# Performance work log

Measured on AMD Instinct MI355X. Metric: run time of the kernel, lower is better.

Reference implementation:

```python
import jax, jax.numpy as jnp
import numpy as np

DG, UF, Z, FD = 32, 4, 16, 16      # decoder grid, upsample factor, z bins, feat dim
H = W = DG * UF                     # 128 BEV resolution
S = 128                             # depth samples per ray
MLP_H = 32
X_MIN, X_MAX = -51.2, 51.2
Y_MIN, Y_MAX = -51.2, 51.2
Z_MIN, Z_MAX = -5.0, 3.0
D_MIN, D_MAX = 1.0, 50.0


def setup_inputs() -> dict:
    key = jax.random.key(0)
    ks = jax.random.split(key, 8)
    B, R, D = 2, 8192, 512
    out_dim = UF * UF * Z * FD
    s1 = 1.0 / np.sqrt(D); s2 = 1.0 / np.sqrt(FD); s3 = 1.0 / np.sqrt(MLP_H)
    return {
        'decoder_output': jax.random.normal(ks[0], (B, DG * DG, D), jnp.float32),
        'ray_origins': jax.random.normal(ks[1], (B, R, 3), jnp.float32),
        'ray_directions': jax.random.normal(ks[2], (B, R, 3), jnp.float32),
        'ln_g': jnp.ones((D,), jnp.float32),
        'ln_b': jnp.zeros((D,), jnp.float32),
        'W1': jax.random.uniform(ks[3], (D, out_dim), jnp.float32, -s1, s1),
        'b1': jnp.zeros((out_dim,), jnp.float32),
        'W2': jax.random.uniform(ks[4], (FD, MLP_H), jnp.float32, -s2, s2),
        'b2': jnp.zeros((MLP_H,), jnp.float32),
        'W3': jax.random.uniform(ks[5], (MLP_H, 1), jnp.float32, -s3, s3),
        'b3': jnp.zeros((1,), jnp.float32),
    }


def _build_nfg(dec, ln_g, ln_b, W1, b1):
    B = dec.shape[0]
    mu = dec.mean(-1, keepdims=True)
    var = dec.var(-1, keepdims=True)  # biased, matches torch LayerNorm
    x = (dec - mu) / jnp.sqrt(var + 1e-5) * ln_g + ln_b
    x = x @ W1 + b1
    x = x.reshape(B, DG, DG, UF, UF, Z, FD).transpose(0, 1, 3, 2, 4, 5, 6)
    x = x.reshape(B, H, W, Z, FD)
    return x.transpose(0, 4, 3, 1, 2)  # (B, F, Z, H, W)


def _trilinear_one(nfg_b, cw, ch, cd):
    # nfg_b: (F, Z, H, W); cw/ch/cd: (P,) in [-1,1] indexing W/H/Z resp.
    # align_corners=True mapping, zeros padding (mask OOB corners).
    fw = (cw + 1.0) * 0.5 * (W - 1)
    fh = (ch + 1.0) * 0.5 * (H - 1)
    fd = (cd + 1.0) * 0.5 * (Z - 1)
    w0 = jnp.floor(fw); h0 = jnp.floor(fh); d0 = jnp.floor(fd)
    tw = fw - w0; th = fh - h0; td = fd - d0
    out = jnp.zeros((nfg_b.shape[0], cw.shape[0]), nfg_b.dtype)
    for dd in (0, 1):
        for hh in (0, 1):
            for ww in (0, 1):
                di = d0 + dd; hi = h0 + hh; wi = w0 + ww
                wt = ((td if dd else 1.0 - td) * (th if hh else 1.0 - th)
                      * (tw if ww else 1.0 - tw))
                valid = ((di >= 0) & (di <= Z - 1) & (hi >= 0) & (hi <= H - 1)
                         & (wi >= 0) & (wi <= W - 1))
                dic = jnp.clip(di, 0, Z - 1).astype(jnp.int32)
                hic = jnp.clip(hi, 0, H - 1).astype(jnp.int32)
                wic = jnp.clip(wi, 0, W - 1).astype(jnp.int32)
                out = out + nfg_b[:, dic, hic, wic] * (wt * valid)
    return out  # (F, P)


def reference(decoder_output, ray_origins, ray_directions,
              ln_g, ln_b, W1, b1, W2, b2, W3, b3):
    nfg = _build_nfg(decoder_output, ln_g, ln_b, W1, b1)  # (B,F,Z,H,W)
    B, R, _ = ray_origins.shape
    t = jnp.linspace(0.0, 1.0, S, dtype=jnp.float32)
    depths = D_MIN + (D_MAX - D_MIN) * t                       # (S,)
    pts = ray_origins[:, :, None, :] + ray_directions[:, :, None, :] * depths[None, None, :, None]
    xn = 2.0 * (pts[..., 0] - X_MIN) / (X_MAX - X_MIN) - 1.0
    yn = 2.0 * (pts[..., 1] - Y_MIN) / (Y_MAX - Y_MIN) - 1.0
    zn = 2.0 * (pts[..., 2] - Z_MIN) / (Z_MAX - Z_MIN) - 1.0
    # torch grid_sample grid last dim = (x,y,z) -> (W,H,D); grid was stacked [y,x,z]
    cw = yn.reshape(B, -1); ch = xn.reshape(B, -1); cd = zn.reshape(B, -1)
    feats = jax.vmap(_trilinear_one)(nfg, cw, ch, cd)          # (B, F, R*S)
    feats = feats.transpose(0, 2, 1).reshape(B, R, S, FD)
    h = jax.nn.relu(feats @ W2 + b2)
    alpha = jax.nn.sigmoid((h @ W3 + b3)[..., 0])              # (B, R, S)
    oma = 1.0 - alpha + 1e-10
    trans = jnp.cumprod(
        jnp.concatenate([jnp.ones((B, R, 1), alpha.dtype), oma[..., :-1]], -1), -1)
    weights = alpha * trans
    pred_depths = (weights * depths[None, None, :]).sum(-1)    # (B, R)
    return pred_depths, weights, nfg
```

## Files before the change

### kernel.cpp

```cpp
#include <hip/hip_runtime.h>
#include <math.h>

#define DG   32
#define UF   4
#define ZB   16
#define FD   16
#define HH   128
#define WWID 128
#define SNUM 128
#define BATCH 2
#define RAYS  8192
#define NTOK  2048
#define DINP  512
#define ODIM  4096
#define MLPH  32

#define OUT_PRED_OFF 0
#define OUT_W_OFF    (BATCH*RAYS)
#define OUT_NFG_OFF  (OUT_W_OFF + BATCH*RAYS*SNUM)

typedef _Float16 half8 __attribute__((ext_vector_type(8)));
typedef _Float16 half4 __attribute__((ext_vector_type(4)));
typedef _Float16 h2 __attribute__((ext_vector_type(2)));
typedef float f32x4 __attribute__((ext_vector_type(4)));

#define GLDS16(gp, lp) \
    __builtin_amdgcn_global_load_lds((const __attribute__((address_space(1))) void*)(gp), \
                                     (__attribute__((address_space(3))) void*)(lp), 16, 0, 0)

__global__ __launch_bounds__(256) void prep_kernel(const float* __restrict__ dec,
                                                   const float* __restrict__ lng,
                                                   const float* __restrict__ lnb,
                                                   const float* __restrict__ W2,
                                                   const float* __restrict__ b2,
                                                   const float* __restrict__ W3,
                                                   const float* __restrict__ W1,
                                                   _Float16* __restrict__ Af,
                                                   _Float16* __restrict__ W1T,
                                                   _Float16* __restrict__ W2f,
                                                   float* __restrict__ b2f,
                                                   float* __restrict__ w3f) {
    int tid = threadIdx.x;
    if (blockIdx.x < NTOK) {
        int t = blockIdx.x;
        const float2* row = reinterpret_cast<const float2*>(dec + (size_t)t * DINP);
        float2 v = row[tid];

        __shared__ float red[4];
        __shared__ float stat[2];

        float s = v.x + v.y;
        #pragma unroll
        for (int o = 32; o > 0; o >>= 1) s += __shfl_down(s, o);
        if ((tid & 63) == 0) red[tid >> 6] = s;
        __syncthreads();
        if (tid == 0) stat[0] = (red[0] + red[1] + red[2] + red[3]) * (1.0f / DINP);
        __syncthreads();
        float mu = stat[0];

        float dx = v.x - mu, dy = v.y - mu;
        float q = dx * dx + dy * dy;
        #pragma unroll
        for (int o = 32; o > 0; o >>= 1) q += __shfl_down(q, o);
        if ((tid & 63) == 0) red[tid >> 6] = q;
        __syncthreads();
        if (tid == 0) {
            float var = (red[0] + red[1] + red[2] + red[3]) * (1.0f / DINP);
            stat[1] = 1.0f / sqrtf(var + 1e-5f);
        }
        __syncthreads();
        float rstd = stat[1];

        int c = 2 * tid;
        h2 o2;
        o2.x = (_Float16)(dx * rstd * lng[c]     + lnb[c]);
        o2.y = (_Float16)(dy * rstd * lng[c + 1] + lnb[c + 1]);
        *reinterpret_cast<h2*>(Af + (size_t)t * DINP + c) = o2;

        if (blockIdx.x == 0 && tid < 128) {
            int jt = tid >> 6, l = tid & 63;
            int sub = l & 15, g = l >> 4;
            #pragma unroll
            for (int e = 0; e < 4; ++e) {
                W2f[(jt * 64 + l) * 4 + e] = (_Float16)W2[(g * 4 + e) * MLPH + jt * 16 + sub];
                b2f[(jt * 64 + l) * 4 + e] = b2[jt * 16 + g * 4 + e];
                w3f[(jt * 64 + l) * 4 + e] = W3[jt * 16 + g * 4 + e];
            }
        }
    } else {
        __shared__ float st[64][65];
        int blk = blockIdx.x - NTOK;
        int c0 = (blk & 63) * 64;
        int k0 = (blk >> 6) * 64;
        {
            int r = tid >> 2, cq = (tid & 3) * 16;
            const float* src = W1 + (size_t)(k0 + r) * ODIM + c0 + cq;
            #pragma unroll
            for (int qq = 0; qq < 4; ++qq) {
                float4 v = *reinterpret_cast<const float4*>(src + qq * 4);
                st[r][cq + qq * 4 + 0] = v.x;
                st[r][cq + qq * 4 + 1] = v.y;
                st[r][cq + qq * 4 + 2] = v.z;
                st[r][cq + qq * 4 + 3] = v.w;
            }
        }
        __syncthreads();
        {
            int cc = tid >> 2, kq = (tid & 3) * 16;
            _Float16 tmp[16];
            #pragma unroll
            for (int i = 0; i < 16; ++i) tmp[i] = (_Float16)st[kq + i][cc];
            _Float16* dst = W1T + (size_t)(c0 + cc) * DINP + k0 + kq;
            *reinterpret_cast<half8*>(dst)     = *reinterpret_cast<half8*>(&tmp[0]);
            *reinterpret_cast<half8*>(dst + 8) = *reinterpret_cast<half8*>(&tmp[8]);
        }
    }
}

__global__ __launch_bounds__(256, 2) void gemm_mfma_kernel(
        const _Float16* __restrict__ Af, const _Float16* __restrict__ W1T,
        const float* __restrict__ bias, _Float16* __restrict__ gh) {
    __shared__ _Float16 As[128 * 32];
    __shared__ _Float16 Bs[128 * 32];

    int tid = threadIdx.x;
    int l = tid & 63, w = tid >> 6;
    int wr = w >> 1, wc = w & 1;
    int row0 = blockIdx.y * 128;
    int col0 = blockIdx.x * 128;

    const char* Ag0 = (const char*)Af + (size_t)(row0 + w * 32 + (l >> 2)) * (DINP * 2) + (l & 3) * 16;
    const char* Ag1 = Ag0 + 16 * (DINP * 2);
    const char* Bg0 = (const char*)W1T + (size_t)(col0 + w * 32 + (l >> 2)) * (DINP * 2) + (l & 3) * 16;
    const char* Bg1 = Bg0 + 16 * (DINP * 2);
    char* lA0 = (char*)As + w * 2048;
    char* lA1 = lA0 + 1024;
    char* lB0 = (char*)Bs + w * 2048;
    char* lB1 = lB0 + 1024;

    f32x4 acc[4][4] = {};

    for (int kk = 0; kk < DINP; kk += 32) {
        GLDS16(Ag0, lA0); GLDS16(Ag1, lA1);
        GLDS16(Bg0, lB0); GLDS16(Bg1, lB1);
        Ag0 += 64; Ag1 += 64; Bg0 += 64; Bg1 += 64;
        __syncthreads();

        half8 af[4], bf[4];
        #pragma unroll
        for (int m = 0; m < 4; ++m)
            af[m] = *reinterpret_cast<const half8*>(As + (wr * 64 + m * 16 + (l & 15)) * 32 + (l >> 4) * 8);
        #pragma unroll
        for (int n = 0; n < 4; ++n)
            bf[n] = *reinterpret_cast<const half8*>(Bs + (wc * 64 + n * 16 + (l & 15)) * 32 + (l >> 4) * 8);
        #pragma unroll
        for (int m = 0; m < 4; ++m)
            #pragma unroll
            for (int n = 0; n < 4; ++n)
                acc[m][n] = __builtin_amdgcn_mfma_f32_16x16x32_f16(af[m], bf[n], acc[m][n], 0, 0, 0);
        __syncthreads();
    }

    #pragma unroll
    for (int n = 0; n < 4; ++n) {
        int c = col0 + wc * 64 + n * 16 + (l & 15);
        float bv = bias[c];
        int f = c & 15, z = (c >> 4) & 15, v = (c >> 8) & 3, u = (c >> 10) & 3;
        #pragma unroll
        for (int m = 0; m < 4; ++m) {
            int rbase = row0 + wr * 64 + m * 16 + ((l >> 4) << 2);
            #pragma unroll
            for (int j = 0; j < 4; ++j) {
                int t = rbase + j;
                int bb = t >> 10;
                int g = t & 1023;
                int i = g >> 5, j2 = g & 31;
                int h = i * 4 + u, wq = j2 * 4 + v;
                size_t gaddr = ((((size_t)(bb * ZB + z) * HH + h) * WWID + wq) << 4) + f;
                gh[gaddr] = (_Float16)(acc[m][n][j] + bv);
            }
        }
    }
}

__device__ __forceinline__ void gather_feat(const _Float16* __restrict__ gb,
                                            float px, float py, float pz,
                                            h2* __restrict__ a) {
    float fw = (py * (1.0f / 51.2f) + 1.0f) * 63.5f;
    float fh = (px * (1.0f / 51.2f) + 1.0f) * 63.5f;
    float fd = (pz + 5.0f) * (0.25f * 7.5f);
    float w0f = floorf(fw), h0f = floorf(fh), d0f = floorf(fd);
    float tw = fw - w0f, th = fh - h0f, td = fd - d0f;
    int w0 = (int)w0f, h0 = (int)h0f, d0 = (int)d0f;

    float aw0 = (w0 >= 0 && w0 <= WWID - 1) ? (1.0f - tw) : 0.0f;
    float aw1 = (w0 + 1 >= 0 && w0 + 1 <= WWID - 1) ? tw : 0.0f;
    float ah0 = (h0 >= 0 && h0 <= HH - 1) ? (1.0f - th) : 0.0f;
    float ah1 = (h0 + 1 >= 0 && h0 + 1 <= HH - 1) ? th : 0.0f;
    float ad0 = (d0 >= 0 && d0 <= ZB - 1) ? (1.0f - td) : 0.0f;
    float ad1 = (d0 + 1 >= 0 && d0 + 1 <= ZB - 1) ? td : 0.0f;

    if ((ad0 + ad1) * (ah0 + ah1) * (aw0 + aw1) <= 0.0f) return;

    int w0c = min(max(w0, 0), WWID - 1), w1c = min(max(w0 + 1, 0), WWID - 1);
    int h0c = min(max(h0, 0), HH - 1),   h1c = min(max(h0 + 1, 0), HH - 1);
    int d0c = min(max(d0, 0), ZB - 1),   d1c = min(max(d0 + 1, 0), ZB - 1);

    int od0 = d0c * (HH * WWID * FD), od1 = d1c * (HH * WWID * FD);
    int oh0 = h0c * (WWID * FD),      oh1 = h1c * (WWID * FD);
    int ow0 = w0c * FD,               ow1 = w1c * FD;

#define CORNER(OFF, WF) do { \
        const uint4* cp_ = reinterpret_cast<const uint4*>(gb + (OFF)); \
        uint4 A_ = cp_[0], B_ = cp_[1]; \
        _Float16 wh_ = (_Float16)(WF); \
        h2 w2_ = {wh_, wh_}; \
        a[0] += __builtin_bit_cast(h2, A_.x) * w2_; \
        a[1] += __builtin_bit_cast(h2, A_.y) * w2_; \
        a[2] += __builtin_bit_cast(h2, A_.z) * w2_; \
        a[3] += __builtin_bit_cast(h2, A_.w) * w2_; \
        a[4] += __builtin_bit_cast(h2, B_.x) * w2_; \
        a[5] += __builtin_bit_cast(h2, B_.y) * w2_; \
        a[6] += __builtin_bit_cast(h2, B_.z) * w2_; \
        a[7] += __builtin_bit_cast(h2, B_.w) * w2_; \
    } while (0)

    CORNER(od0 + oh0 + ow0, ad0 * ah0 * aw0);
    CORNER(od0 + oh0 + ow1, ad0 * ah0 * aw1);
    CORNER(od0 + oh1 + ow0, ad0 * ah1 * aw0);
    CORNER(od0 + oh1 + ow1, ad0 * ah1 * aw1);
    CORNER(od1 + oh0 + ow0, ad1 * ah0 * aw0);
    CORNER(od1 + oh0 + ow1, ad1 * ah0 * aw1);
    CORNER(od1 + oh1 + ow0, ad1 * ah1 * aw0);
    CORNER(od1 + oh1 + ow1, ad1 * ah1 * aw1);
#undef CORNER
}

#define SF 24
#define RAYBLK (BATCH * RAYS / 4)
__global__ __launch_bounds__(256) void consume_kernel(
        const float* __restrict__ orig, const float* __restrict__ dirs,
        const _Float16* __restrict__ gh,
        const _Float16* __restrict__ W2f, const float* __restrict__ b2f,
        const float* __restrict__ w3f, const float* __restrict__ b3,
        float* __restrict__ pred_out, float* __restrict__ w_out,
        float* __restrict__ nfg) {
    __shared__ __align__(16) char smem[4 * 128 * SF * 2];
    int tid = threadIdx.x;
    int bx = blockIdx.x;

    if ((bx & 1) == 0) {
        _Float16* featLDS = reinterpret_cast<_Float16*>(smem);
        int lane = tid & 63, wvid = tid >> 6;
        int ray = (bx >> 1) * 4 + wvid;
        int bb = ray >> 13;

        _Float16* FL = &featLDS[wvid * 128 * SF];

        const float* o3 = orig + (size_t)ray * 3;
        const float* d3 = dirs + (size_t)ray * 3;
        float ox = o3[0], oy = o3[1], oz = o3[2];
        float dx = d3[0], dy = d3[1], dz = d3[2];

        const _Float16* gb = gh + (size_t)bb * (ZB * HH * WWID * FD);

        float t0 = 1.0f + 49.0f * ((float)lane * (1.0f / 127.0f));
        float t1 = 1.0f + 49.0f * ((float)(lane + 64) * (1.0f / 127.0f));

        h2 acc0[8] = {}, acc1[8] = {};
        gather_feat(gb, ox + dx * t0, oy + dy * t0, oz + dz * t0, acc0);
        gather_feat(gb, ox + dx * t1, oy + dy * t1, oz + dz * t1, acc1);

        {
            uint4 p0, p1;
            p0.x = __builtin_bit_cast(unsigned int, acc0[0]);
            p0.y = __builtin_bit_cast(unsigned int, acc0[1]);
            p0.z = __builtin_bit_cast(unsigned int, acc0[2]);
            p0.w = __builtin_bit_cast(unsigned int, acc0[3]);
            p1.x = __builtin_bit_cast(unsigned int, acc0[4]);
            p1.y = __builtin_bit_cast(unsigned int, acc0[5]);
            p1.z = __builtin_bit_cast(unsigned int, acc0[6]);
            p1.w = __builtin_bit_cast(unsigned int, acc0[7]);
            *reinterpret_cast<uint4*>(FL + lane * SF)     = p0;
            *reinterpret_cast<uint4*>(FL + lane * SF + 8) = p1;
            uint4 q0, q1;
            q0.x = __builtin_bit_cast(unsigned int, acc1[0]);
            q0.y = __builtin_bit_cast(unsigned int, acc1[1]);
            q0.z = __builtin_bit_cast(unsigned int, acc1[2]);
            q0.w = __builtin_bit_cast(unsigned int, acc1[3]);
            q1.x = __builtin_bit_cast(unsigned int, acc1[4]);
            q1.y = __builtin_bit_cast(unsigned int, acc1[5]);
            q1.z = __builtin_bit_cast(unsigned int, acc1[6]);
            q1.w = __builtin_bit_cast(unsigned int, acc1[7]);
            *reinterpret_cast<uint4*>(FL + (lane + 64) * SF)     = q0;
            *reinterpret_cast<uint4*>(FL + (lane + 64) * SF + 8) = q1;
        }

        half4 Af0 = *reinterpret_cast<const half4*>(W2f + lane * 4);
        half4 Af1 = *reinterpret_cast<const half4*>(W2f + (64 + lane) * 4);
        f32x4 b20 = *reinterpret_cast<const f32x4*>(b2f + lane * 4);
        f32x4 b21 = *reinterpret_cast<const f32x4*>(b2f + (64 + lane) * 4);
        f32x4 w30 = *reinterpret_cast<const f32x4*>(w3f + lane * 4);
        f32x4 w31 = *reinterpret_cast<const f32x4*>(w3f + (64 + lane) * 4);
        float b3v = b3[0];

        float at[8];
        #pragma unroll
        for (int tt = 0; tt < 8; ++tt) {
            half4 bfrag = *reinterpret_cast<const half4*>(
                FL + (tt * 16 + (lane & 15)) * SF + (lane >> 4) * 4);
            f32x4 c0 = __builtin_amdgcn_mfma_f32_16x16x16f16(Af0, bfrag, b20, 0, 0, 0);
            f32x4 c1 = __builtin_amdgcn_mfma_f32_16x16x16f16(Af1, bfrag, b21, 0, 0, 0);
            float p = 0.0f;
            #pragma unroll
            for (int r = 0; r < 4; ++r) {
                p = fmaf(fmaxf(c0[r], 0.0f), w30[r], p);
                p = fmaf(fmaxf(c1[r], 0.0f), w31[r], p);
            }
            p += __shfl_xor(p, 16);
            p += __shfl_xor(p, 32);
            at[tt] = p;
        }
        int g2 = lane >> 4;
        float aS0 = at[0];
        aS0 = (g2 == 1) ? at[1] : aS0;
        aS0 = (g2 == 2) ? at[2] : aS0;
        aS0 = (g2 == 3) ? at[3] : aS0;
        float aS1 = at[4];
        aS1 = (g2 == 1) ? at[5] : aS1;
        aS1 = (g2 == 2) ? at[6] : aS1;
        aS1 = (g2 == 3) ? at[7] : aS1;
        aS0 += b3v; aS1 += b3v;

        float alpha0 = 1.0f / (1.0f + __expf(-aS0));
        float alpha1 = 1.0f / (1.0f + __expf(-aS1));
        float oma0 = 1.0f - alpha0 + 1e-10f;
        float oma1 = 1.0f - alpha1 + 1e-10f;

        float P = oma0;
        #pragma unroll
        for (int off = 1; off < 64; off <<= 1) {
            float u = __shfl_up(P, off);
            if (lane >= off) P *= u;
        }
        float T64 = __shfl(P, 63);
        float Q = oma1;
        #pragma unroll
        for (int off = 1; off < 64; off <<= 1) {
            float u = __shfl_up(Q, off);
            if (lane >= off) Q *= u;
        }
        float e0 = __shfl_up(P, 1);
        if (lane == 0) e0 = 1.0f;
        float e1 = __shfl_up(Q, 1);
        e1 = (lane == 0) ? T64 : e1 * T64;

        float w0 = alpha0 * e0;
        float w1 = alpha1 * e1;
        w_out[(size_t)ray * SNUM + lane] = w0;
        w_out[(size_t)ray * SNUM + 64 + lane] = w1;

        float pv = w0 * t0 + w1 * t1;
        #pragma unroll
        for (int o = 32; o > 0; o >>= 1) pv += __shfl_xor(pv, o);
        if (lane == 0) pred_out[ray] = pv;
    } else {
        float* sl = reinterpret_cast<float*>(smem);
        int blk = bx >> 1;
        int bb = blk >> 11, z = (blk >> 7) & 15, h = blk & 127;
        const uint4* src = reinterpret_cast<const uint4*>(gh + (size_t)blk * 2048);
        uint4 v = src[tid];
        int wv = tid >> 1, fb = (tid & 1) * 8;
        h2 p0 = __builtin_bit_cast(h2, v.x);
        h2 p1 = __builtin_bit_cast(h2, v.y);
        h2 p2 = __builtin_bit_cast(h2, v.z);
        h2 p3 = __builtin_bit_cast(h2, v.w);
        float* sr = &sl[wv * 17 + fb];
        sr[0] = (float)p0.x; sr[1] = (float)p0.y;
        sr[2] = (float)p1.x; sr[3] = (float)p1.y;
        sr[4] = (float)p2.x; sr[5] = (float)p2.y;
        sr[6] = (float)p3.x; sr[7] = (float)p3.y;
        __syncthreads();
        int f = tid >> 4, w0 = (tid & 15) * 8;
        float* dst = nfg + (((size_t)(bb * FD + f) * ZB + z) * (HH * WWID)) + h * WWID + w0;
        float4 o0, o1;
        o0.x = sl[(w0 + 0) * 17 + f]; o0.y = sl[(w0 + 1) * 17 + f];
        o0.z = sl[(w0 + 2) * 17 + f]; o0.w = sl[(w0 + 3) * 17 + f];
        o1.x = sl[(w0 + 4) * 17 + f]; o1.y = sl[(w0 + 5) * 17 + f];
        o1.z = sl[(w0 + 6) * 17 + f]; o1.w = sl[(w0 + 7) * 17 + f];
        *reinterpret_cast<float4*>(dst) = o0;
        *reinterpret_cast<float4*>(dst + 4) = o1;
    }
}

extern "C" void kernel_launch(void* const* d_in, const int* in_sizes, int n_in,
                              void* d_out, int out_size, void* d_ws, size_t ws_size,
                              hipStream_t stream) {
    const float* dec = (const float*)d_in[0];
    const float* ro  = (const float*)d_in[1];
    const float* rd  = (const float*)d_in[2];
    const float* lng = (const float*)d_in[3];
    const float* lnb = (const float*)d_in[4];
    const float* W1  = (const float*)d_in[5];
    const float* b1  = (const float*)d_in[6];
    const float* W2  = (const float*)d_in[7];
    const float* b2  = (const float*)d_in[8];
    const float* W3  = (const float*)d_in[9];
    const float* b3  = (const float*)d_in[10];

    float* out = (float*)d_out;
    char*  wsb = (char*)d_ws;
    _Float16* Af  = (_Float16*)wsb;
    _Float16* W1T = (_Float16*)(wsb + (2u << 20));
    _Float16* gh  = (_Float16*)(wsb + (6u << 20));
    _Float16* W2f = (_Float16*)(wsb + (23u << 20));
    float*    b2f = (float*)(wsb + (23u << 20) + 4096);
    float*    w3f = (float*)(wsb + (23u << 20) + 8192);

    prep_kernel<<<NTOK + (ODIM / 64) * (DINP / 64), 256, 0, stream>>>(
        dec, lng, lnb, W2, b2, W3, W1, Af, W1T, W2f, b2f, w3f);

    dim3 gg(ODIM / 128, NTOK / 128);
    gemm_mfma_kernel<<<gg, 256, 0, stream>>>(Af, W1T, b1, gh);

    consume_kernel<<<2 * RAYBLK, 256, 0, stream>>>(ro, rd, gh, W2f, b2f, w3f, b3,
                                                   out + OUT_PRED_OFF, out + OUT_W_OFF,
                                                   out + OUT_NFG_OFF);
}
```

Baseline: 71.85 us.

## Split NFG transpose into own kernel, pair W-corner loads, halve feature LDS

The interleaved consume kernel is split into a dedicated ray kernel and a separate transpose kernel that writes the NFG output, launched after it. Trilinear gathering now loads the two W-neighbour corners as one contiguous 64-byte read from a clamped base index, with the weights remapped at the borders. Features for the two sample halves are staged through a half-size LDS buffer in turn, which lowers LDS use per block and may raise occupancy. The cost is an extra kernel launch and no more overlap between the transpose and ray work.

Result: faster. 63.57 us (-11.5%).

```diff
diff --git a/kernel.cpp b/kernel.cpp
--- a/kernel.cpp
+++ b/kernel.cpp
@@ -183,6 +183,36 @@
     }
 }
 
+__global__ __launch_bounds__(256) void tp_kernel(const _Float16* __restrict__ gh,
+                                                 float* __restrict__ nfg) {
+    int blk = blockIdx.x;
+    int bb = blk >> 11, z = (blk >> 7) & 15, h = blk & 127;
+    __shared__ float sl[128 * 17];
+    int tid = threadIdx.x;
+    const uint4* src = reinterpret_cast<const uint4*>(gh + (size_t)blk * 2048);
+    uint4 v = src[tid];
+    int wv = tid >> 1, fb = (tid & 1) * 8;
+    h2 p0 = __builtin_bit_cast(h2, v.x);
+    h2 p1 = __builtin_bit_cast(h2, v.y);
+    h2 p2 = __builtin_bit_cast(h2, v.z);
+    h2 p3 = __builtin_bit_cast(h2, v.w);
+    float* sr = &sl[wv * 17 + fb];
+    sr[0] = (float)p0.x; sr[1] = (float)p0.y;
+    sr[2] = (float)p1.x; sr[3] = (float)p1.y;
+    sr[4] = (float)p2.x; sr[5] = (float)p2.y;
+    sr[6] = (float)p3.x; sr[7] = (float)p3.y;
+    __syncthreads();
+    int f = tid >> 4, w0 = (tid & 15) * 8;
+    float* dst = nfg + (((size_t)(bb * FD + f) * ZB + z) * (HH * WWID)) + h * WWID + w0;
+    float4 o0, o1;
+    o0.x = sl[(w0 + 0) * 17 + f]; o0.y = sl[(w0 + 1) * 17 + f];
+    o0.z = sl[(w0 + 2) * 17 + f]; o0.w = sl[(w0 + 3) * 17 + f];
+    o1.x = sl[(w0 + 4) * 17 + f]; o1.y = sl[(w0 + 5) * 17 + f];
+    o1.z = sl[(w0 + 6) * 17 + f]; o1.w = sl[(w0 + 7) * 17 + f];
+    *reinterpret_cast<float4*>(dst) = o0;
+    *reinterpret_cast<float4*>(dst + 4) = o1;
+}
+
 __device__ __forceinline__ void gather_feat(const _Float16* __restrict__ gb,
                                             float px, float py, float pz,
                                             h2* __restrict__ a) {
@@ -202,111 +232,100 @@
 
     if ((ad0 + ad1) * (ah0 + ah1) * (aw0 + aw1) <= 0.0f) return;
 
-    int w0c = min(max(w0, 0), WWID - 1), w1c = min(max(w0 + 1, 0), WWID - 1);
     int h0c = min(max(h0, 0), HH - 1),   h1c = min(max(h0 + 1, 0), HH - 1);
     int d0c = min(max(d0, 0), ZB - 1),   d1c = min(max(d0 + 1, 0), ZB - 1);
+    int wb = min(max(w0, 0), WWID - 2);
+    float ws0 = (wb == w0) ? aw0 : ((wb == w0 + 1) ? aw1 : 0.0f);
+    float ws1 = (wb == w0) ? aw1 : ((wb == w0 - 1) ? aw0 : 0.0f);
 
     int od0 = d0c * (HH * WWID * FD), od1 = d1c * (HH * WWID * FD);
     int oh0 = h0c * (WWID * FD),      oh1 = h1c * (WWID * FD);
-    int ow0 = w0c * FD,               ow1 = w1c * FD;
-
-#define CORNER(OFF, WF) do { \
+    int ow  = wb * FD;
+
+#define CPAIR(OFF, WDH) do { \
         const uint4* cp_ = reinterpret_cast<const uint4*>(gb + (OFF)); \
-        uint4 A_ = cp_[0], B_ = cp_[1]; \
-        _Float16 wh_ = (_Float16)(WF); \
-        h2 w2_ = {wh_, wh_}; \
-        a[0] += __builtin_bit_cast(h2, A_.x) * w2_; \
-        a[1] += __builtin_bit_cast(h2, A_.y) * w2_; \
-        a[2] += __builtin_bit_cast(h2, A_.z) * w2_; \
-        a[3] += __builtin_bit_cast(h2, A_.w) * w2_; \
-        a[4] += __builtin_bit_cast(h2, B_.x) * w2_; \
-        a[5] += __builtin_bit_cast(h2, B_.y) * w2_; \
-        a[6] += __builtin_bit_cast(h2, B_.z) * w2_; \
-        a[7] += __builtin_bit_cast(h2, B_.w) * w2_; \
+        uint4 A_ = cp_[0], B_ = cp_[1], C_ = cp_[2], D_ = cp_[3]; \
+        _Float16 u0_ = (_Float16)((WDH) * ws0); \
+        _Float16 u1_ = (_Float16)((WDH) * ws1); \
+        h2 W0_ = {u0_, u0_}; h2 W1_ = {u1_, u1_}; \
+        a[0] += __builtin_bit_cast(h2, A_.x) * W0_; \
+        a[1] += __builtin_bit_cast(h2, A_.y) * W0_; \
+        a[2] += __builtin_bit_cast(h2, A_.z) * W0_; \
+        a[3] += __builtin_bit_cast(h2, A_.w) * W0_; \
+        a[4] += __builtin_bit_cast(h2, B_.x) * W0_; \
+        a[5] += __builtin_bit_cast(h2, B_.y) * W0_; \
+        a[6] += __builtin_bit_cast(h2, B_.z) * W0_; \
+        a[7] += __builtin_bit_cast(h2, B_.w) * W0_; \
+        a[0] += __builtin_bit_cast(h2, C_.x) * W1_; \
+        a[1] += __builtin_bit_cast(h2, C_.y) * W1_; \
+        a[2] += __builtin_bit_cast(h2, C_.z) * W1_; \
+        a[3] += __builtin_bit_cast(h2, C_.w) * W1_; \
+        a[4] += __builtin_bit_cast(h2, D_.x) * W1_; \
+        a[5] += __builtin_bit_cast(h2, D_.y) * W1_; \
+        a[6] += __builtin_bit_cast(h2, D_.z) * W1_; \
+        a[7] += __builtin_bit_cast(h2, D_.w) * W1_; \
     } while (0)
 
-    CORNER(od0 + oh0 + ow0, ad0 * ah0 * aw0);
-    CORNER(od0 + oh0 + ow1, ad0 * ah0 * aw1);
-    CORNER(od0 + oh1 + ow0, ad0 * ah1 * aw0);
-    CORNER(od0 + oh1 + ow1, ad0 * ah1 * aw1);
-    CORNER(od1 + oh0 + ow0, ad1 * ah0 * aw0);
-    CORNER(od1 + oh0 + ow1, ad1 * ah0 * aw1);
-    CORNER(od1 + oh1 + ow0, ad1 * ah1 * aw0);
-    CORNER(od1 + oh1 + ow1, ad1 * ah1 * aw1);
-#undef CORNER
+    CPAIR(od0 + oh0 + ow, ad0 * ah0);
+    CPAIR(od0 + oh1 + ow, ad0 * ah1);
+    CPAIR(od1 + oh0 + ow, ad1 * ah0);
+    CPAIR(od1 + oh1 + ow, ad1 * ah1);
+#undef CPAIR
 }
 
 #define SF 24
-#define RAYBLK (BATCH * RAYS / 4)
-__global__ __launch_bounds__(256) void consume_kernel(
+__global__ __launch_bounds__(256) void ray_fused_kernel(
         const float* __restrict__ orig, const float* __restrict__ dirs,
         const _Float16* __restrict__ gh,
         const _Float16* __restrict__ W2f, const float* __restrict__ b2f,
         const float* __restrict__ w3f, const float* __restrict__ b3,
-        float* __restrict__ pred_out, float* __restrict__ w_out,
-        float* __restrict__ nfg) {
-    __shared__ __align__(16) char smem[4 * 128 * SF * 2];
+        float* __restrict__ pred_out, float* __restrict__ w_out) {
     int tid = threadIdx.x;
-    int bx = blockIdx.x;
-
-    if ((bx & 1) == 0) {
-        _Float16* featLDS = reinterpret_cast<_Float16*>(smem);
-        int lane = tid & 63, wvid = tid >> 6;
-        int ray = (bx >> 1) * 4 + wvid;
-        int bb = ray >> 13;
-
-        _Float16* FL = &featLDS[wvid * 128 * SF];
-
-        const float* o3 = orig + (size_t)ray * 3;
-        const float* d3 = dirs + (size_t)ray * 3;
-        float ox = o3[0], oy = o3[1], oz = o3[2];
-        float dx = d3[0], dy = d3[1], dz = d3[2];
-
-        const _Float16* gb = gh + (size_t)bb * (ZB * HH * WWID * FD);
-
-        float t0 = 1.0f + 49.0f * ((float)lane * (1.0f / 127.0f));
-        float t1 = 1.0f + 49.0f * ((float)(lane + 64) * (1.0f / 127.0f));
-
-        h2 acc0[8] = {}, acc1[8] = {};
-        gather_feat(gb, ox + dx * t0, oy + dy * t0, oz + dz * t0, acc0);
-        gather_feat(gb, ox + dx * t1, oy + dy * t1, oz + dz * t1, acc1);
-
-        {
-            uint4 p0, p1;
-            p0.x = __builtin_bit_cast(unsigned int, acc0[0]);
-            p0.y = __builtin_bit_cast(unsigned int, acc0[1]);
-            p0.z = __builtin_bit_cast(unsigned int, acc0[2]);
-            p0.w = __builtin_bit_cast(unsigned int, acc0[3]);
-            p1.x = __builtin_bit_cast(unsigned int, acc0[4]);
-            p1.y = __builtin_bit_cast(unsigned int, acc0[5]);
-            p1.z = __builtin_bit_cast(unsigned int, acc0[6]);
-            p1.w = __builtin_bit_cast(unsigned int, acc0[7]);
-            *reinterpret_cast<uint4*>(FL + lane * SF)     = p0;
-            *reinterpret_cast<uint4*>(FL + lane * SF + 8) = p1;
-            uint4 q0, q1;
-            q0.x = __builtin_bit_cast(unsigned int, acc1[0]);
-            q0.y = __builtin_bit_cast(unsigned int, acc1[1]);
-            q0.z = __builtin_bit_cast(unsigned int, acc1[2]);
-            q0.w = __builtin_bit_cast(unsigned int, acc1[3]);
-            q1.x = __builtin_bit_cast(unsigned int, acc1[4]);
-            q1.y = __builtin_bit_cast(unsigned int, acc1[5]);
-            q1.z = __builtin_bit_cast(unsigned int, acc1[6]);
-            q1.w = __builtin_bit_cast(unsigned int, acc1[7]);
-            *reinterpret_cast<uint4*>(FL + (lane + 64) * SF)     = q0;
-            *reinterpret_cast<uint4*>(FL + (lane + 64) * SF + 8) = q1;
-        }
-
-        half4 Af0 = *reinterpret_cast<const half4*>(W2f + lane * 4);
-        half4 Af1 = *reinterpret_cast<const half4*>(W2f + (64 + lane) * 4);
-        f32x4 b20 = *reinterpret_cast<const f32x4*>(b2f + lane * 4);
-        f32x4 b21 = *reinterpret_cast<const f32x4*>(b2f + (64 + lane) * 4);
-        f32x4 w30 = *reinterpret_cast<const f32x4*>(w3f + lane * 4);
-        f32x4 w31 = *reinterpret_cast<const f32x4*>(w3f + (64 + lane) * 4);
-        float b3v = b3[0];
-
-        float at[8];
-        #pragma unroll
-        for (int tt = 0; tt < 8; ++tt) {
+    int lane = tid & 63, wvid = tid >> 6;
+    int ray = blockIdx.x * 4 + wvid;
+    int bb = ray >> 13;
+
+    __shared__ _Float16 featLDS[4 * 64 * SF];
+    _Float16* FL = &featLDS[wvid * 64 * SF];
+
+    const float* o3 = orig + (size_t)ray * 3;
+    const float* d3 = dirs + (size_t)ray * 3;
+    float ox = o3[0], oy = o3[1], oz = o3[2];
+    float dx = d3[0], dy = d3[1], dz = d3[2];
+
+    const _Float16* gb = gh + (size_t)bb * (ZB * HH * WWID * FD);
+
+    float t0 = 1.0f + 49.0f * ((float)lane * (1.0f / 127.0f));
+    float t1 = 1.0f + 49.0f * ((float)(lane + 64) * (1.0f / 127.0f));
+
+    h2 acc0[8] = {}, acc1[8] = {};
+    gather_feat(gb, ox + dx * t0, oy + dy * t0, oz + dz * t0, acc0);
+    gather_feat(gb, ox + dx * t1, oy + dy * t1, oz + dz * t1, acc1);
+
+    half4 Af0 = *reinterpret_cast<const half4*>(W2f + lane * 4);
+    half4 Af1 = *reinterpret_cast<const half4*>(W2f + (64 + lane) * 4);
+    f32x4 b20 = *reinterpret_cast<const f32x4*>(b2f + lane * 4);
+    f32x4 b21 = *reinterpret_cast<const f32x4*>(b2f + (64 + lane) * 4);
+    f32x4 w30 = *reinterpret_cast<const f32x4*>(w3f + lane * 4);
+    f32x4 w31 = *reinterpret_cast<const f32x4*>(w3f + (64 + lane) * 4);
+    float b3v = b3[0];
+
+    float at[8];
+
+    {
+        uint4 p0, p1;
+        p0.x = __builtin_bit_cast(unsigned int, acc0[0]);
+        p0.y = __builtin_bit_cast(unsigned int, acc0[1]);
+        p0.z = __builtin_bit_cast(unsigned int, acc0[2]);
+        p0.w = __builtin_bit_cast(unsigned int, acc0[3]);
+        p1.x = __builtin_bit_cast(unsigned int, acc0[4]);
+        p1.y = __builtin_bit_cast(unsigned int, acc0[5]);
+        p1.z = __builtin_bit_cast(unsigned int, acc0[6]);
+        p1.w = __builtin_bit_cast(unsigned int, acc0[7]);
+        *reinterpret_cast<uint4*>(FL + lane * SF)     = p0;
+        *reinterpret_cast<uint4*>(FL + lane * SF + 8) = p1;
+        #pragma unroll
+        for (int tt = 0; tt < 4; ++tt) {
             half4 bfrag = *reinterpret_cast<const half4*>(
                 FL + (tt * 16 + (lane & 15)) * SF + (lane >> 4) * 4);
             f32x4 c0 = __builtin_amdgcn_mfma_f32_16x16x16f16(Af0, bfrag, b20, 0, 0, 0);
@@ -321,76 +340,80 @@
             p += __shfl_xor(p, 32);
             at[tt] = p;
         }
-        int g2 = lane >> 4;
-        float aS0 = at[0];
-        aS0 = (g2 == 1) ? at[1] : aS0;
-        aS0 = (g2 == 2) ? at[2] : aS0;
-        aS0 = (g2 == 3) ? at[3] : aS0;
-        float aS1 = at[4];
-        aS1 = (g2 == 1) ? at[5] : aS1;
-        aS1 = (g2 == 2) ? at[6] : aS1;
-        aS1 = (g2 == 3) ? at[7] : aS1;
-        aS0 += b3v; aS1 += b3v;
-
-        float alpha0 = 1.0f / (1.0f + __expf(-aS0));
-        float alpha1 = 1.0f / (1.0f + __expf(-aS1));
-        float oma0 = 1.0f - alpha0 + 1e-10f;
-        float oma1 = 1.0f - alpha1 + 1e-10f;
-
-        float P = oma0;
-        #pragma unroll
-        for (int off = 1; off < 64; off <<= 1) {
-            float u = __shfl_up(P, off);
-            if (lane >= off) P *= u;
-        }
-        float T64 = __shfl(P, 63);
-        float Q = oma1;
-        #pragma unroll
-        for (int off = 1; off < 64; off <<= 1) {
-            float u = __shfl_up(Q, off);
-            if (lane >= off) Q *= u;
-        }
-        float e0 = __shfl_up(P, 1);
-        if (lane == 0) e0 = 1.0f;
-        float e1 = __shfl_up(Q, 1);
-        e1 = (lane == 0) ? T64 : e1 * T64;
-
-        float w0 = alpha0 * e0;
-        float w1 = alpha1 * e1;
-        w_out[(size_t)ray * SNUM + lane] = w0;
-        w_out[(size_t)ray * SNUM + 64 + lane] = w1;
-
-        float pv = w0 * t0 + w1 * t1;
-        #pragma unroll
-        for (int o = 32; o > 0; o >>= 1) pv += __shfl_xor(pv, o);
-        if (lane == 0) pred_out[ray] = pv;
-    } else {
-        float* sl = reinterpret_cast<float*>(smem);
-        int blk = bx >> 1;
-        int bb = blk >> 11, z = (blk >> 7) & 15, h = blk & 127;
-        const uint4* src = reinterpret_cast<const uint4*>(gh + (size_t)blk * 2048);
-        uint4 v = src[tid];
-        int wv = tid >> 1, fb = (tid & 1) * 8;
-        h2 p0 = __builtin_bit_cast(h2, v.x);
-        h2 p1 = __builtin_bit_cast(h2, v.y);
-        h2 p2 = __builtin_bit_cast(h2, v.z);
-        h2 p3 = __builtin_bit_cast(h2, v.w);
-        float* sr = &sl[wv * 17 + fb];
-        sr[0] = (float)p0.x; sr[1] = (float)p0.y;
-        sr[2] = (float)p1.x; sr[3] = (float)p1.y;
-        sr[4] = (float)p2.x; sr[5] = (float)p2.y;
-        sr[6] = (float)p3.x; sr[7] = (float)p3.y;
-        __syncthreads();
-        int f = tid >> 4, w0 = (tid & 15) * 8;
-        float* dst = nfg + (((size_t)(bb * FD + f) * ZB + z) * (HH * WWID)) + h * WWID + w0;
-        float4 o0, o1;
-        o0.x = sl[(w0 + 0) * 17 + f]; o0.y = sl[(w0 + 1) * 17 + f];
-        o0.z = sl[(w0 + 2) * 17 + f]; o0.w = sl[(w0 + 3) * 17 + f];
-        o1.x = sl[(w0 + 4) * 17 + f]; o1.y = sl[(w0 + 5) * 17 + f];
-        o1.z = sl[(w0 + 6) * 17 + f]; o1.w = sl[(w0 + 7) * 17 + f];
-        *reinterpret_cast<float4*>(dst) = o0;
-        *reinterpret_cast<float4*>(dst + 4) = o1;
-    }
+    }
+    {
+        uint4 q0, q1;
+        q0.x = __builtin_bit_cast(unsigned int, acc1[0]);
+        q0.y = __builtin_bit_cast(unsigned int, acc1[1]);
+        q0.z = __builtin_bit_cast(unsigned int, acc1[2]);
+        q0.w = __builtin_bit_cast(unsigned int, acc1[3]);
+        q1.x = __builtin_bit_cast(unsigned int, acc1[4]);
+        q1.y = __builtin_bit_cast(unsigned int, acc1[5]);
+        q1.z = __builtin_bit_cast(unsigned int, acc1[6]);
+        q1.w = __builtin_bit_cast(unsigned int, acc1[7]);
+        *reinterpret_cast<uint4*>(FL + lane * SF)     = q0;
+        *reinterpret_cast<uint4*>(FL + lane * SF + 8) = q1;
+        #pragma unroll
+        for (int tt = 0; tt < 4; ++tt) {
+            half4 bfrag = *reinterpret_cast<const half4*>(
+                FL + (tt * 16 + (lane & 15)) * SF + (lane >> 4) * 4);
+            f32x4 c0 = __builtin_amdgcn_mfma_f32_16x16x16f16(Af0, bfrag, b20, 0, 0, 0);
+            f32x4 c1 = __builtin_amdgcn_mfma_f32_16x16x16f16(Af1, bfrag, b21, 0, 0, 0);
+            float p = 0.0f;
+            #pragma unroll
+            for (int r = 0; r < 4; ++r) {
+                p = fmaf(fmaxf(c0[r], 0.0f), w30[r], p);
+                p = fmaf(fmaxf(c1[r], 0.0f), w31[r], p);
+            }
+            p += __shfl_xor(p, 16);
+            p += __shfl_xor(p, 32);
+            at[tt + 4] = p;
+        }
+    }
+
+    int g2 = lane >> 4;
+    float aS0 = at[0];
+    aS0 = (g2 == 1) ? at[1] : aS0;
+    aS0 = (g2 == 2) ? at[2] : aS0;
+    aS0 = (g2 == 3) ? at[3] : aS0;
+    float aS1 = at[4];
+    aS1 = (g2 == 1) ? at[5] : aS1;
+    aS1 = (g2 == 2) ? at[6] : aS1;
+    aS1 = (g2 == 3) ? at[7] : aS1;
+    aS0 += b3v; aS1 += b3v;
+
+    float alpha0 = 1.0f / (1.0f + __expf(-aS0));
+    float alpha1 = 1.0f / (1.0f + __expf(-aS1));
+    float oma0 = 1.0f - alpha0 + 1e-10f;
+    float oma1 = 1.0f - alpha1 + 1e-10f;
+
+    float P = oma0;
+    #pragma unroll
+    for (int off = 1; off < 64; off <<= 1) {
+        float u = __shfl_up(P, off);
+        if (lane >= off) P *= u;
+    }
+    float T64 = __shfl(P, 63);
+    float Q = oma1;
+    #pragma unroll
+    for (int off = 1; off < 64; off <<= 1) {
+        float u = __shfl_up(Q, off);
+        if (lane >= off) Q *= u;
+    }
+    float e0 = __shfl_up(P, 1);
+    if (lane == 0) e0 = 1.0f;
+    float e1 = __shfl_up(Q, 1);
+    e1 = (lane == 0) ? T64 : e1 * T64;
+
+    float w0 = alpha0 * e0;
+    float w1 = alpha1 * e1;
+    w_out[(size_t)ray * SNUM + lane] = w0;
+    w_out[(size_t)ray * SNUM + 64 + lane] = w1;
+
+    float pv = w0 * t0 + w1 * t1;
+    #pragma unroll
+    for (int o = 32; o > 0; o >>= 1) pv += __shfl_xor(pv, o);
+    if (lane == 0) pred_out[ray] = pv;
 }
 
 extern "C" void kernel_launch(void* const* d_in, const int* in_sizes, int n_in,
@@ -423,7 +446,8 @@
     dim3 gg(ODIM / 128, NTOK / 128);
     gemm_mfma_kernel<<<gg, 256, 0, stream>>>(Af, W1T, b1, gh);
 
-    consume_kernel<<<2 * RAYBLK, 256, 0, stream>>>(ro, rd, gh, W2f, b2f, w3f, b3,
-                                                   out + OUT_PRED_OFF, out + OUT_W_OFF,
-                                                   out + OUT_NFG_OFF);
-}
+    ray_fused_kernel<<<BATCH * RAYS / 4, 256, 0, stream>>>(ro, rd, gh, W2f, b2f, w3f, b3,
+                                                           out + OUT_PRED_OFF, out + OUT_W_OFF);
+
+    tp_kernel<<<BATCH * ZB * HH, 256, 0, stream>>>(gh, out + OUT_NFG_OFF);
+}
```
